# Performance work log

Measured on AMD Instinct MI355X. Metric: run time of the kernel, lower is better.

## Reference

```python
import jax, jax.numpy as jnp
import numpy as np

B, H, W, D, K = 32, 64, 64, 128, 1024

def setup_inputs() -> dict:
    key = jax.random.key(0)
    k1, k2 = jax.random.split(key)
    inputs = jax.random.normal(k1, (B, H, W, D), dtype=jnp.float32)
    embedding = jax.random.normal(k2, (D, K), dtype=jnp.float32)  # codebook, column per code
    return {"inputs": inputs, "embedding": embedding}

def reference(inputs, embedding):
    D_ = embedding.shape[0]
    x = inputs.reshape(-1, D_)                                  # [N, D]
    dist = (jnp.sum(x * x, axis=-1, keepdims=True)
            - 2.0 * (x @ embedding)
            + jnp.sum(embedding * embedding, axis=0, keepdims=True))  # [N, K]
    idx = jnp.argmax(-dist, axis=1).reshape(inputs.shape[:-1])  # [B, H, W]
    return embedding.T[idx]                                     # [B, H, W, D]
```

## Files before the change

kernel.cpp:

```cpp
#include <hip/hip_runtime.h>

#define KC 1024
#define DD 128
#define NT_COUNT (KC / 16)
#define RPB 64

typedef short bf16x8 __attribute__((ext_vector_type(8)));
typedef float f32x4  __attribute__((ext_vector_type(4)));

#define AS1 __attribute__((address_space(1)))
#define AS3 __attribute__((address_space(3)))

static __device__ __forceinline__ unsigned short f2bf(float f) {
    unsigned u = __float_as_uint(f);
    unsigned r = (u + 0x7fffu + ((u >> 16) & 1u)) >> 16;
    return (unsigned short)r;
}
static __device__ __forceinline__ float bf2f(unsigned short h) {
    return __uint_as_float(((unsigned)h) << 16);
}
static __device__ __forceinline__ void gl_lds16(const void* g, void* l) {
    __builtin_amdgcn_global_load_lds((const AS1 void*)g, (AS3 void*)l, 16, 0, 0);
}
static __device__ __forceinline__ void gl_lds4(const void* g, void* l) {
    __builtin_amdgcn_global_load_lds((const AS1 void*)g, (AS3 void*)l, 4, 0, 0);
}

__global__ __launch_bounds__(256) void vq_prep(const float* __restrict__ E,
                                               float* __restrict__ e2h,
                                               float* __restrict__ ET,
                                               unsigned short* __restrict__ Bpk) {
    __shared__ float T[16 * 129];
    const int nt  = blockIdx.x;
    const int tid = threadIdx.x;

    for (int i = tid; i < 16 * DD; i += 256) {
        int d  = i >> 4;
        int kk = i & 15;
        T[kk * 129 + d] = E[(size_t)d * KC + nt * 16 + kk];
    }
    __syncthreads();

    if (tid < 16) {
        float s = 0.f;
#pragma unroll 16
        for (int d = 0; d < DD; ++d) {
            float v = T[tid * 129 + d];
            s = fmaf(v, v, s);
        }
        e2h[nt * 16 + tid] = 512.0f - 0.5f * s;
    }

    for (int i = tid; i < 16 * DD; i += 256) {
        int kk = i >> 7;
        int d  = i & 127;
        ET[(size_t)(nt * 16 + kk) * DD + d] = T[kk * 129 + d];
    }

    {
        const int s    = tid >> 6;
        const int lane = tid & 63;
        const int kk   = lane & 15;
        const int d0   = s * 32 + (lane >> 4) * 8;
        bf16x8 hi, lo;
#pragma unroll
        for (int j = 0; j < 8; ++j) {
            float v = T[kk * 129 + d0 + j];
            unsigned short h = f2bf(v);
            hi[j] = (short)h;
            lo[j] = (short)f2bf(v - bf2f(h));
        }
        char* base = (char*)Bpk + (size_t)nt * 8192 + s * 1024 + lane * 16;
        *(bf16x8*)(base)        = hi;
        *(bf16x8*)(base + 4096) = lo;
    }
}

__global__ __launch_bounds__(64, 2) void vq_main(const float* __restrict__ X,
                                                 const float* __restrict__ e2h,
                                                 const float* __restrict__ ET,
                                                 const unsigned short* __restrict__ Bpk,
                                                 float* __restrict__ Out) {
    __shared__ __align__(16) char lds[2 * 8448];
    int*   s_k1  = (int*)(lds);
    int*   s_k2  = (int*)(lds + 256);
    int*   s_win = (int*)(lds + 512);
    float* s_gap = (float*)(lds + 768);

    const int lane  = threadIdx.x;
    const int quad  = lane >> 4;
    const int n16   = lane & 15;
    const int wrow0 = blockIdx.x * RPB;
    const int lidx16 = lane * 16;
    const int lidx4  = lane * 4;

    bf16x8 ahi[4][4], alo[4][4];
#pragma unroll
    for (int t = 0; t < 4; ++t) {
#pragma unroll
        for (int s = 0; s < 4; ++s) {
            const int row = wrow0 + t * 16 + n16;
            const int d0  = s * 32 + quad * 8;
            const float4 p = *(const float4*)(X + (size_t)row * DD + d0);
            const float4 q = *(const float4*)(X + (size_t)row * DD + d0 + 4);
            float v[8] = {p.x, p.y, p.z, p.w, q.x, q.y, q.z, q.w};
#pragma unroll
            for (int j = 0; j < 8; ++j) {
                unsigned short h = f2bf(v[j]);
                ahi[t][s][j] = (short)h;
                alo[t][s][j] = (short)f2bf(v[j] - bf2f(h));
            }
        }
    }

    float p1[4][4], p2[4][4];
#pragma unroll
    for (int t = 0; t < 4; ++t)
#pragma unroll
        for (int r = 0; r < 4; ++r) { p1[t][r] = 0.0f; p2[t][r] = 0.0f; }

#define STAGE(NT, BOFF)                                                          \
    do {                                                                         \
        const char* g = (const char*)Bpk + (size_t)(NT) * 8192;                  \
        _Pragma("unroll")                                                        \
        for (int c = 0; c < 8; ++c)                                              \
            gl_lds16(g + c * 1024 + lidx16, lds + (BOFF) + c * 1024);            \
        gl_lds4(e2h + (NT) * 16 + n16, lds + (BOFF) + 8192);                     \
    } while (0)

#define TILE(NT, BOFF)                                                           \
    do {                                                                         \
        const char* l = lds + (BOFF);                                            \
        const bf16x8 bh0 = *(const bf16x8*)(l + 0 * 1024 + lidx16);              \
        const bf16x8 bh1 = *(const bf16x8*)(l + 1 * 1024 + lidx16);              \
        const bf16x8 bh2 = *(const bf16x8*)(l + 2 * 1024 + lidx16);              \
        const bf16x8 bh3 = *(const bf16x8*)(l + 3 * 1024 + lidx16);              \
        const bf16x8 bl0 = *(const bf16x8*)(l + 4 * 1024 + lidx16);              \
        const bf16x8 bl1 = *(const bf16x8*)(l + 5 * 1024 + lidx16);              \
        const bf16x8 bl2 = *(const bf16x8*)(l + 6 * 1024 + lidx16);              \
        const bf16x8 bl3 = *(const bf16x8*)(l + 7 * 1024 + lidx16);              \
        const float  ev  = *(const float*)(l + 8192 + lidx4);                    \
        const unsigned ntinv = (unsigned)(63 - (NT));                            \
        _Pragma("unroll")                                                        \
        for (int t = 0; t < 4; ++t) {                                            \
            f32x4 aA = {ev, ev, ev, ev};                                         \
            f32x4 aB = {0.f, 0.f, 0.f, 0.f};                                     \
            f32x4 aC = {0.f, 0.f, 0.f, 0.f};                                     \
            aA = __builtin_amdgcn_mfma_f32_16x16x32_bf16(ahi[t][0], bh0, aA, 0, 0, 0); \
            aB = __builtin_amdgcn_mfma_f32_16x16x32_bf16(alo[t][0], bh0, aB, 0, 0, 0); \
            aC = __builtin_amdgcn_mfma_f32_16x16x32_bf16(ahi[t][0], bl0, aC, 0, 0, 0); \
            aA = __builtin_amdgcn_mfma_f32_16x16x32_bf16(ahi[t][1], bh1, aA, 0, 0, 0); \
            aB = __builtin_amdgcn_mfma_f32_16x16x32_bf16(alo[t][1], bh1, aB, 0, 0, 0); \
            aC = __builtin_amdgcn_mfma_f32_16x16x32_bf16(ahi[t][1], bl1, aC, 0, 0, 0); \
            aA = __builtin_amdgcn_mfma_f32_16x16x32_bf16(ahi[t][2], bh2, aA, 0, 0, 0); \
            aB = __builtin_amdgcn_mfma_f32_16x16x32_bf16(alo[t][2], bh2, aB, 0, 0, 0); \
            aC = __builtin_amdgcn_mfma_f32_16x16x32_bf16(ahi[t][2], bl2, aC, 0, 0, 0); \
            aA = __builtin_amdgcn_mfma_f32_16x16x32_bf16(ahi[t][3], bh3, aA, 0, 0, 0); \
            aB = __builtin_amdgcn_mfma_f32_16x16x32_bf16(alo[t][3], bh3, aB, 0, 0, 0); \
            aC = __builtin_amdgcn_mfma_f32_16x16x32_bf16(ahi[t][3], bl3, aC, 0, 0, 0); \
            _Pragma("unroll")                                                    \
            for (int r = 0; r < 4; ++r) {                                        \
                float sv = (aA[r] + aB[r]) + aC[r];                              \
                float v = __uint_as_float((__float_as_uint(sv) & ~63u) | ntinv); \
                float lo = fminf(p1[t][r], v);                                   \
                p1[t][r] = fmaxf(p1[t][r], v);                                   \
                p2[t][r] = fmaxf(p2[t][r], lo);                                  \
            }                                                                    \
        }                                                                        \
    } while (0)

    STAGE(0, 0);
    for (int nt = 0; nt < NT_COUNT; nt += 2) {
        STAGE(nt + 1, 8448);
        __builtin_amdgcn_s_waitcnt(3961);
        __builtin_amdgcn_sched_barrier(0);
        TILE(nt, 0);
        if (nt + 2 < NT_COUNT) {
            STAGE(nt + 2, 0);
            __builtin_amdgcn_s_waitcnt(3961);
        } else {
            __builtin_amdgcn_s_waitcnt(3952);
        }
        __builtin_amdgcn_sched_barrier(0);
        TILE(nt + 1, 8448);
    }
#undef STAGE
#undef TILE

#pragma unroll
    for (int t = 0; t < 4; ++t) {
#pragma unroll
        for (int r = 0; r < 4; ++r) {
            unsigned u1 = __float_as_uint(p1[t][r]);
            unsigned u2 = __float_as_uint(p2[t][r]);
            int k1 = (int)(63u - (u1 & 63u)) * 16 + n16;
            int k2 = (int)(63u - (u2 & 63u)) * 16 + n16;
            unsigned long long q1 =
                ((unsigned long long)(u1 & ~63u) << 32) | (unsigned)(1023 - k1);
            unsigned long long q2 =
                ((unsigned long long)(u2 & ~63u) << 32) | (unsigned)(1023 - k2);
#pragma unroll
            for (int m = 1; m < 16; m <<= 1) {
                unsigned long long o1 = __shfl_xor(q1, m, 64);
                unsigned long long o2 = __shfl_xor(q2, m, 64);
                unsigned long long lo = q1 < o1 ? q1 : o1;
                q1 = q1 > o1 ? q1 : o1;
                unsigned long long hi2 = q2 > o2 ? q2 : o2;
                q2 = lo > hi2 ? lo : hi2;
            }
            if (n16 == 0) {
                int row = t * 16 + quad * 4 + r;
                s_k1[row] = 1023 - (int)(q1 & 1023u);
                s_k2[row] = 1023 - (int)(q2 & 1023u);
                s_gap[row] = __uint_as_float((unsigned)(q1 >> 32)) -
                             __uint_as_float((unsigned)(q2 >> 32));
            }
        }
    }
    __syncthreads();

    {
        const int k1 = s_k1[lane];
        const int k2 = s_k2[lane];
        int win = k1;
        if (s_gap[lane] < 0.5f) {
            const float4* __restrict__ xr  = (const float4*)(X + (size_t)(wrow0 + lane) * DD);
            const float4* __restrict__ e1  = (const float4*)(ET + (size_t)k1 * DD);
            const float4* __restrict__ e2p = (const float4*)(ET + (size_t)k2 * DD);
            double dot1 = 0.0, ee1 = 0.0, dot2 = 0.0, ee2 = 0.0;
#pragma unroll 4
            for (int d4 = 0; d4 < DD / 4; ++d4) {
                const float4 xv = xr[d4];
                const float4 v1 = e1[d4];
                const float4 v2 = e2p[d4];
                const float xs[4] = {xv.x, xv.y, xv.z, xv.w};
                const float a1[4] = {v1.x, v1.y, v1.z, v1.w};
                const float a2[4] = {v2.x, v2.y, v2.z, v2.w};
#pragma unroll
                for (int j = 0; j < 4; ++j) {
                    const double xd  = (double)xs[j];
                    const double v1d = (double)a1[j];
                    const double v2d = (double)a2[j];
                    dot1 = fma(xd, v1d, dot1);
                    ee1  = fma(v1d, v1d, ee1);
                    dot2 = fma(xd, v2d, dot2);
                    ee2  = fma(v2d, v2d, ee2);
                }
            }
            double d1 = ee1 - 2.0 * dot1;
            double d2 = ee2 - 2.0 * dot2;
            win = (d2 < d1 || (d2 == d1 && k2 < k1)) ? k2 : k1;
        }
        s_win[lane] = win;
    }
    __syncthreads();

    for (int i = lane; i < RPB * (DD / 4); i += 64) {
        const int row = i >> 5;
        const int d4  = i & 31;
        const float4 v = *(const float4*)(ET + (size_t)s_win[row] * DD + d4 * 4);
        *(float4*)(Out + (size_t)(wrow0 + row) * DD + d4 * 4) = v;
    }
}

extern "C" void kernel_launch(void* const* d_in, const int* in_sizes, int n_in,
                              void* d_out, int out_size, void* d_ws, size_t ws_size,
                              hipStream_t stream) {
    const float* X = (const float*)d_in[0];
    const float* E = (const float*)d_in[1];
    float* Out = (float*)d_out;

    float* e2h = (float*)d_ws;
    float* ET  = e2h + KC;
    unsigned short* Bpk = (unsigned short*)(ET + (size_t)KC * DD);

    const int N = in_sizes[0] / DD;

    hipLaunchKernelGGL(vq_prep, dim3(NT_COUNT), dim3(256), 0, stream, E, e2h, ET, Bpk);
    hipLaunchKernelGGL(vq_main, dim3(N / RPB), dim3(64), 0, stream,
                       X, e2h, ET, Bpk, Out);
}
```

Baseline: 216.8 us.

## Triple-buffer codebook tiles, preload code norms into LDS, raise MFMA priority

The main loop moves from double to triple buffering of the packed bf16 codebook tiles, so two tiles are in flight while one is computed, with matching vmcnt waits. The per-tile 4-byte global-to-LDS load of the code norms is replaced by a single upfront copy of all 1024 norms into LDS. s_setprio is raised around the MFMA block. The goal is to hide more global load latency at the cost of extra LDS per block, which could reduce occupancy.

```diff
diff --git a/kernel.cpp b/kernel.cpp
--- a/kernel.cpp
+++ b/kernel.cpp
@@ -11,6 +11,10 @@
 #define AS1 __attribute__((address_space(1)))
 #define AS3 __attribute__((address_space(3)))
 
+#define VMC16 20336
+#define VMC8  3960
+#define VMC0  3952
+
 static __device__ __forceinline__ unsigned short f2bf(float f) {
     unsigned u = __float_as_uint(f);
     unsigned r = (u + 0x7fffu + ((u >> 16) & 1u)) >> 16;
@@ -21,9 +25,6 @@
 }
 static __device__ __forceinline__ void gl_lds16(const void* g, void* l) {
     __builtin_amdgcn_global_load_lds((const AS1 void*)g, (AS3 void*)l, 16, 0, 0);
-}
-static __device__ __forceinline__ void gl_lds4(const void* g, void* l) {
-    __builtin_amdgcn_global_load_lds((const AS1 void*)g, (AS3 void*)l, 4, 0, 0);
 }
 
 __global__ __launch_bounds__(256) void vq_prep(const float* __restrict__ E,
@@ -81,7 +82,8 @@
                                                  const float* __restrict__ ET,
                                                  const unsigned short* __restrict__ Bpk,
                                                  float* __restrict__ Out) {
-    __shared__ __align__(16) char lds[2 * 8448];
+    __shared__ __align__(16) char lds[3 * 8192 + 4096];
+    float* s_e2  = (float*)(lds + 24576);
     int*   s_k1  = (int*)(lds);
     int*   s_k2  = (int*)(lds + 256);
     int*   s_win = (int*)(lds + 512);
@@ -92,7 +94,6 @@
     const int n16   = lane & 15;
     const int wrow0 = blockIdx.x * RPB;
     const int lidx16 = lane * 16;
-    const int lidx4  = lane * 4;
 
     bf16x8 ahi[4][4], alo[4][4];
 #pragma unroll
@@ -113,23 +114,28 @@
         }
     }
 
+    for (int i = lane; i < KC; i += 64) s_e2[i] = e2h[i];
+    __syncthreads();
+
     float p1[4][4], p2[4][4];
 #pragma unroll
     for (int t = 0; t < 4; ++t)
 #pragma unroll
         for (int r = 0; r < 4; ++r) { p1[t][r] = 0.0f; p2[t][r] = 0.0f; }
 
-#define STAGE(NT, BOFF)                                                          \
+#define STAGE(T, BOFF)                                                           \
     do {                                                                         \
-        const char* g = (const char*)Bpk + (size_t)(NT) * 8192;                  \
+        const char* g = (const char*)Bpk + (size_t)(T) * 8192;                   \
         _Pragma("unroll")                                                        \
         for (int c = 0; c < 8; ++c)                                              \
             gl_lds16(g + c * 1024 + lidx16, lds + (BOFF) + c * 1024);            \
-        gl_lds4(e2h + (NT) * 16 + n16, lds + (BOFF) + 8192);                     \
     } while (0)
 
-#define TILE(NT, BOFF)                                                           \
+#define BODY(T, BOFF, STG, SBOFF, WENC)                                          \
     do {                                                                         \
+        if (STG) STAGE((T) + 2, SBOFF);                                          \
+        __builtin_amdgcn_s_waitcnt(WENC);                                        \
+        __builtin_amdgcn_sched_barrier(0);                                       \
         const char* l = lds + (BOFF);                                            \
         const bf16x8 bh0 = *(const bf16x8*)(l + 0 * 1024 + lidx16);              \
         const bf16x8 bh1 = *(const bf16x8*)(l + 1 * 1024 + lidx16);              \
@@ -139,8 +145,9 @@
         const bf16x8 bl1 = *(const bf16x8*)(l + 5 * 1024 + lidx16);              \
         const bf16x8 bl2 = *(const bf16x8*)(l + 6 * 1024 + lidx16);              \
         const bf16x8 bl3 = *(const bf16x8*)(l + 7 * 1024 + lidx16);              \
-        const float  ev  = *(const float*)(l + 8192 + lidx4);                    \
-        const unsigned ntinv = (unsigned)(63 - (NT));                            \
+        const float  ev  = s_e2[(T) * 16 + n16];                                 \
+        const unsigned ntinv = (unsigned)(63 - (T));                             \
+        __builtin_amdgcn_s_setprio(1);                                           \
         _Pragma("unroll")                                                        \
         for (int t = 0; t < 4; ++t) {                                            \
             f32x4 aA = {ev, ev, ev, ev};                                         \
@@ -167,25 +174,22 @@
                 p2[t][r] = fmaxf(p2[t][r], lo);                                  \
             }                                                                    \
         }                                                                        \
+        __builtin_amdgcn_s_setprio(0);                                           \
     } while (0)
 
     STAGE(0, 0);
-    for (int nt = 0; nt < NT_COUNT; nt += 2) {
-        STAGE(nt + 1, 8448);
-        __builtin_amdgcn_s_waitcnt(3961);
-        __builtin_amdgcn_sched_barrier(0);
-        TILE(nt, 0);
-        if (nt + 2 < NT_COUNT) {
-            STAGE(nt + 2, 0);
-            __builtin_amdgcn_s_waitcnt(3961);
-        } else {
-            __builtin_amdgcn_s_waitcnt(3952);
-        }
-        __builtin_amdgcn_sched_barrier(0);
-        TILE(nt + 1, 8448);
-    }
+    STAGE(1, 8192);
+    for (int nt = 0; nt < 60; nt += 3) {
+        BODY(nt,     0,     1, 16384, VMC16);
+        BODY(nt + 1, 8192,  1, 0,     VMC16);
+        BODY(nt + 2, 16384, 1, 8192,  VMC16);
+    }
+    BODY(60, 0,     1, 16384, VMC16);
+    BODY(61, 8192,  1, 0,     VMC16);
+    BODY(62, 16384, 0, 0,     VMC8);
+    BODY(63, 0,     0, 0,     VMC0);
+#undef BODY
 #undef STAGE
-#undef TILE
 
 #pragma unroll
     for (int t = 0; t < 4; ++t) {
```

Measured after the change: 276.4 us. 27.5% more time.

## Load codebook tiles directly into registers instead of async global-to-LDS staging

Applied to the files above, without the earlier changes.

Replaces the global_load_lds double-buffered staging of packed bf16 codebook tiles with plain global loads into two register buffers, leaving the compiler to schedule the waits. The e2 norms are now preloaded once into LDS for all codes rather than staged per tile. This drops the LDS round trip and the manual waitcnt/sched_barrier control, at the cost of 16 extra bf16x8 registers per lane, which may cut occupancy or add spills, and it relies on compiler-inserted waits to overlap loads with the MFMAs.

```diff
diff --git a/kernel.cpp b/kernel.cpp
--- a/kernel.cpp
+++ b/kernel.cpp
@@ -8,9 +8,6 @@
 typedef short bf16x8 __attribute__((ext_vector_type(8)));
 typedef float f32x4  __attribute__((ext_vector_type(4)));
 
-#define AS1 __attribute__((address_space(1)))
-#define AS3 __attribute__((address_space(3)))
-
 static __device__ __forceinline__ unsigned short f2bf(float f) {
     unsigned u = __float_as_uint(f);
     unsigned r = (u + 0x7fffu + ((u >> 16) & 1u)) >> 16;
@@ -18,12 +15,6 @@
 }
 static __device__ __forceinline__ float bf2f(unsigned short h) {
     return __uint_as_float(((unsigned)h) << 16);
-}
-static __device__ __forceinline__ void gl_lds16(const void* g, void* l) {
-    __builtin_amdgcn_global_load_lds((const AS1 void*)g, (AS3 void*)l, 16, 0, 0);
-}
-static __device__ __forceinline__ void gl_lds4(const void* g, void* l) {
-    __builtin_amdgcn_global_load_lds((const AS1 void*)g, (AS3 void*)l, 4, 0, 0);
 }
 
 __global__ __launch_bounds__(256) void vq_prep(const float* __restrict__ E,
@@ -81,18 +72,17 @@
                                                  const float* __restrict__ ET,
                                                  const unsigned short* __restrict__ Bpk,
                                                  float* __restrict__ Out) {
-    __shared__ __align__(16) char lds[2 * 8448];
-    int*   s_k1  = (int*)(lds);
-    int*   s_k2  = (int*)(lds + 256);
-    int*   s_win = (int*)(lds + 512);
-    float* s_gap = (float*)(lds + 768);
+    __shared__ float s_e2[KC];
+    __shared__ int   s_k1[RPB];
+    __shared__ int   s_k2[RPB];
+    __shared__ int   s_win[RPB];
+    __shared__ float s_gap[RPB];
 
     const int lane  = threadIdx.x;
     const int quad  = lane >> 4;
     const int n16   = lane & 15;
     const int wrow0 = blockIdx.x * RPB;
     const int lidx16 = lane * 16;
-    const int lidx4  = lane * 4;
 
     bf16x8 ahi[4][4], alo[4][4];
 #pragma unroll
@@ -113,51 +103,44 @@
         }
     }
 
+    for (int i = lane; i < KC; i += 64) s_e2[i] = e2h[i];
+    __syncthreads();
+
     float p1[4][4], p2[4][4];
 #pragma unroll
     for (int t = 0; t < 4; ++t)
 #pragma unroll
         for (int r = 0; r < 4; ++r) { p1[t][r] = 0.0f; p2[t][r] = 0.0f; }
 
-#define STAGE(NT, BOFF)                                                          \
+#define LOADB(NT, BUF)                                                           \
     do {                                                                         \
-        const char* g = (const char*)Bpk + (size_t)(NT) * 8192;                  \
+        const char* g = (const char*)Bpk + (size_t)(NT) * 8192 + lidx16;         \
         _Pragma("unroll")                                                        \
         for (int c = 0; c < 8; ++c)                                              \
-            gl_lds16(g + c * 1024 + lidx16, lds + (BOFF) + c * 1024);            \
-        gl_lds4(e2h + (NT) * 16 + n16, lds + (BOFF) + 8192);                     \
+            BUF[c] = *(const bf16x8*)(g + c * 1024);                             \
     } while (0)
 
-#define TILE(NT, BOFF)                                                           \
+#define TILE(NT, BUF)                                                            \
     do {                                                                         \
-        const char* l = lds + (BOFF);                                            \
-        const bf16x8 bh0 = *(const bf16x8*)(l + 0 * 1024 + lidx16);              \
-        const bf16x8 bh1 = *(const bf16x8*)(l + 1 * 1024 + lidx16);              \
-        const bf16x8 bh2 = *(const bf16x8*)(l + 2 * 1024 + lidx16);              \
-        const bf16x8 bh3 = *(const bf16x8*)(l + 3 * 1024 + lidx16);              \
-        const bf16x8 bl0 = *(const bf16x8*)(l + 4 * 1024 + lidx16);              \
-        const bf16x8 bl1 = *(const bf16x8*)(l + 5 * 1024 + lidx16);              \
-        const bf16x8 bl2 = *(const bf16x8*)(l + 6 * 1024 + lidx16);              \
-        const bf16x8 bl3 = *(const bf16x8*)(l + 7 * 1024 + lidx16);              \
-        const float  ev  = *(const float*)(l + 8192 + lidx4);                    \
+        const float ev = s_e2[(NT) * 16 + n16];                                  \
         const unsigned ntinv = (unsigned)(63 - (NT));                            \
         _Pragma("unroll")                                                        \
         for (int t = 0; t < 4; ++t) {                                            \
             f32x4 aA = {ev, ev, ev, ev};                                         \
             f32x4 aB = {0.f, 0.f, 0.f, 0.f};                                     \
             f32x4 aC = {0.f, 0.f, 0.f, 0.f};                                     \
-            aA = __builtin_amdgcn_mfma_f32_16x16x32_bf16(ahi[t][0], bh0, aA, 0, 0, 0); \
-            aB = __builtin_amdgcn_mfma_f32_16x16x32_bf16(alo[t][0], bh0, aB, 0, 0, 0); \
-            aC = __builtin_amdgcn_mfma_f32_16x16x32_bf16(ahi[t][0], bl0, aC, 0, 0, 0); \
-            aA = __builtin_amdgcn_mfma_f32_16x16x32_bf16(ahi[t][1], bh1, aA, 0, 0, 0); \
-            aB = __builtin_amdgcn_mfma_f32_16x16x32_bf16(alo[t][1], bh1, aB, 0, 0, 0); \
-            aC = __builtin_amdgcn_mfma_f32_16x16x32_bf16(ahi[t][1], bl1, aC, 0, 0, 0); \
-            aA = __builtin_amdgcn_mfma_f32_16x16x32_bf16(ahi[t][2], bh2, aA, 0, 0, 0); \
-            aB = __builtin_amdgcn_mfma_f32_16x16x32_bf16(alo[t][2], bh2, aB, 0, 0, 0); \
-            aC = __builtin_amdgcn_mfma_f32_16x16x32_bf16(ahi[t][2], bl2, aC, 0, 0, 0); \
-            aA = __builtin_amdgcn_mfma_f32_16x16x32_bf16(ahi[t][3], bh3, aA, 0, 0, 0); \
-            aB = __builtin_amdgcn_mfma_f32_16x16x32_bf16(alo[t][3], bh3, aB, 0, 0, 0); \
-            aC = __builtin_amdgcn_mfma_f32_16x16x32_bf16(ahi[t][3], bl3, aC, 0, 0, 0); \
+            aA = __builtin_amdgcn_mfma_f32_16x16x32_bf16(ahi[t][0], BUF[0], aA, 0, 0, 0); \
+            aB = __builtin_amdgcn_mfma_f32_16x16x32_bf16(alo[t][0], BUF[0], aB, 0, 0, 0); \
+            aC = __builtin_amdgcn_mfma_f32_16x16x32_bf16(ahi[t][0], BUF[4], aC, 0, 0, 0); \
+            aA = __builtin_amdgcn_mfma_f32_16x16x32_bf16(ahi[t][1], BUF[1], aA, 0, 0, 0); \
+            aB = __builtin_amdgcn_mfma_f32_16x16x32_bf16(alo[t][1], BUF[1], aB, 0, 0, 0); \
+            aC = __builtin_amdgcn_mfma_f32_16x16x32_bf16(ahi[t][1], BUF[5], aC, 0, 0, 0); \
+            aA = __builtin_amdgcn_mfma_f32_16x16x32_bf16(ahi[t][2], BUF[2], aA, 0, 0, 0); \
+            aB = __builtin_amdgcn_mfma_f32_16x16x32_bf16(alo[t][2], BUF[2], aB, 0, 0, 0); \
+            aC = __builtin_amdgcn_mfma_f32_16x16x32_bf16(ahi[t][2], BUF[6], aC, 0, 0, 0); \
+            aA = __builtin_amdgcn_mfma_f32_16x16x32_bf16(ahi[t][3], BUF[3], aA, 0, 0, 0); \
+            aB = __builtin_amdgcn_mfma_f32_16x16x32_bf16(alo[t][3], BUF[3], aB, 0, 0, 0); \
+            aC = __builtin_amdgcn_mfma_f32_16x16x32_bf16(ahi[t][3], BUF[7], aC, 0, 0, 0); \
             _Pragma("unroll")                                                    \
             for (int r = 0; r < 4; ++r) {                                        \
                 float sv = (aA[r] + aB[r]) + aC[r];                              \
@@ -169,22 +152,15 @@
         }                                                                        \
     } while (0)
 
-    STAGE(0, 0);
+    bf16x8 bufA[8], bufB[8];
+    LOADB(0, bufA);
     for (int nt = 0; nt < NT_COUNT; nt += 2) {
-        STAGE(nt + 1, 8448);
-        __builtin_amdgcn_s_waitcnt(3961);
-        __builtin_amdgcn_sched_barrier(0);
-        TILE(nt, 0);
-        if (nt + 2 < NT_COUNT) {
-            STAGE(nt + 2, 0);
-            __builtin_amdgcn_s_waitcnt(3961);
-        } else {
-            __builtin_amdgcn_s_waitcnt(3952);
-        }
-        __builtin_amdgcn_sched_barrier(0);
-        TILE(nt + 1, 8448);
-    }
-#undef STAGE
+        LOADB(nt + 1, bufB);
+        TILE(nt, bufA);
+        if (nt + 2 < NT_COUNT) LOADB(nt + 2, bufA);
+        TILE(nt + 1, bufB);
+    }
+#undef LOADB
 #undef TILE
 
 #pragma unroll
```

New measurement: 267.1 us. +23.2%, slower.

## Drop codebook low-part MFMA, use certified top-4 with error-bound rescoring

Applied to the files above, without the earlier changes.

Removes the third bf16 MFMA (x_hi times e_lo) from the split-precision distance product, so each tile issues two MFMA chains instead of three and stages half as much codebook data in LDS. To keep argmin exact, it computes per-tile error bounds on the dropped codebook low part in the prep kernel and keeps a top-4 candidate list per row. A row is accepted only when a gap between consecutive candidates exceeds a bound derived from ||x|| and those error bounds; candidates above the gap are rescored in double precision. Rows that fail all gaps fall back to a full double-precision scan over all 1024 codes. This adds heavier top-4 tracking, a serial per-row candidate merge, and the risk of slow fallbacks.

```diff
diff --git a/kernel.cpp b/kernel.cpp
--- a/kernel.cpp
+++ b/kernel.cpp
@@ -7,6 +7,7 @@
 
 typedef short bf16x8 __attribute__((ext_vector_type(8)));
 typedef float f32x4  __attribute__((ext_vector_type(4)));
+typedef unsigned long long u64;
 
 #define AS1 __attribute__((address_space(1)))
 #define AS3 __attribute__((address_space(3)))
@@ -28,9 +29,11 @@
 
 __global__ __launch_bounds__(256) void vq_prep(const float* __restrict__ E,
                                                float* __restrict__ e2h,
+                                               float* __restrict__ gtab,
                                                float* __restrict__ ET,
                                                unsigned short* __restrict__ Bpk) {
     __shared__ float T[16 * 129];
+    __shared__ float red[32];
     const int nt  = blockIdx.x;
     const int tid = threadIdx.x;
 
@@ -42,13 +45,25 @@
     __syncthreads();
 
     if (tid < 16) {
-        float s = 0.f;
+        float s = 0.f, g = 0.f;
 #pragma unroll 16
         for (int d = 0; d < DD; ++d) {
             float v = T[tid * 129 + d];
             s = fmaf(v, v, s);
+            float lo = v - bf2f(f2bf(v));
+            g = fmaf(lo, lo, g);
         }
         e2h[nt * 16 + tid] = 512.0f - 0.5f * s;
+        red[tid] = g;
+        red[16 + tid] = s;
+    }
+    __syncthreads();
+    if (tid == 0) {
+        float mg = 0.f, ms = 0.f;
+#pragma unroll
+        for (int i = 0; i < 16; ++i) { mg = fmaxf(mg, red[i]); ms = fmaxf(ms, red[16 + i]); }
+        gtab[nt] = mg;
+        gtab[64 + nt] = ms;
     }
 
     for (int i = tid; i < 16 * DD; i += 256) {
@@ -58,34 +73,30 @@
     }
 
     {
-        const int s    = tid >> 6;
+        const int c    = tid >> 6;
         const int lane = tid & 63;
         const int kk   = lane & 15;
-        const int d0   = s * 32 + (lane >> 4) * 8;
-        bf16x8 hi, lo;
-#pragma unroll
-        for (int j = 0; j < 8; ++j) {
-            float v = T[kk * 129 + d0 + j];
-            unsigned short h = f2bf(v);
-            hi[j] = (short)h;
-            lo[j] = (short)f2bf(v - bf2f(h));
-        }
-        char* base = (char*)Bpk + (size_t)nt * 8192 + s * 1024 + lane * 16;
-        *(bf16x8*)(base)        = hi;
-        *(bf16x8*)(base + 4096) = lo;
+        const int d0   = c * 32 + (lane >> 4) * 8;
+        bf16x8 hi;
+#pragma unroll
+        for (int j = 0; j < 8; ++j) hi[j] = (short)f2bf(T[kk * 129 + d0 + j]);
+        *(bf16x8*)((char*)Bpk + (size_t)nt * 4096 + c * 1024 + lane * 16) = hi;
     }
 }
 
 __global__ __launch_bounds__(64, 2) void vq_main(const float* __restrict__ X,
                                                  const float* __restrict__ e2h,
+                                                 const float* __restrict__ gtab,
                                                  const float* __restrict__ ET,
                                                  const unsigned short* __restrict__ Bpk,
                                                  float* __restrict__ Out) {
-    __shared__ __align__(16) char lds[2 * 8448];
-    int*   s_k1  = (int*)(lds);
-    int*   s_k2  = (int*)(lds + 256);
-    int*   s_win = (int*)(lds + 512);
-    float* s_gap = (float*)(lds + 768);
+    __shared__ __align__(16) char lds[11008];
+    float* s_xn   = (float*)(lds + 8704);
+    int*   s_cand = (int*)(lds + 8960);
+    int*   s_dep  = (int*)(lds + 9984);
+    int*   s_win  = (int*)(lds + 10240);
+    int*   s_nfs  = (int*)(lds + 10496);
+    int*   s_fsl  = (int*)(lds + 10500);
 
     const int lane  = threadIdx.x;
     const int quad  = lane >> 4;
@@ -94,7 +105,17 @@
     const int lidx16 = lane * 16;
     const int lidx4  = lane * 4;
 
+    float g1 = gtab[lane];
+    float g2 = gtab[64 + lane];
+#pragma unroll
+    for (int m = 1; m < 64; m <<= 1) {
+        g1 = fmaxf(g1, __shfl_xor(g1, m, 64));
+        g2 = fmaxf(g2, __shfl_xor(g2, m, 64));
+    }
+    const float Ecoef = sqrtf(g1) * 1.001f + 8.2e-6f * sqrtf(g2);
+
     bf16x8 ahi[4][4], alo[4][4];
+    float psum[4] = {0.f, 0.f, 0.f, 0.f};
 #pragma unroll
     for (int t = 0; t < 4; ++t) {
 #pragma unroll
@@ -106,26 +127,36 @@
             float v[8] = {p.x, p.y, p.z, p.w, q.x, q.y, q.z, q.w};
 #pragma unroll
             for (int j = 0; j < 8; ++j) {
+                psum[t] = fmaf(v[j], v[j], psum[t]);
                 unsigned short h = f2bf(v[j]);
                 ahi[t][s][j] = (short)h;
                 alo[t][s][j] = (short)f2bf(v[j] - bf2f(h));
             }
         }
     }
-
-    float p1[4][4], p2[4][4];
+#pragma unroll
+    for (int t = 0; t < 4; ++t) {
+        psum[t] += __shfl_xor(psum[t], 16, 64);
+        psum[t] += __shfl_xor(psum[t], 32, 64);
+    }
+    if (quad == 0)
+#pragma unroll
+        for (int t = 0; t < 4; ++t) s_xn[t * 16 + n16] = psum[t];
+    if (lane == 0) *s_nfs = 0;
+
+    float p1[4][4], p2[4][4], p3[4][4], p4[4][4];
 #pragma unroll
     for (int t = 0; t < 4; ++t)
 #pragma unroll
-        for (int r = 0; r < 4; ++r) { p1[t][r] = 0.0f; p2[t][r] = 0.0f; }
+        for (int r = 0; r < 4; ++r) { p1[t][r] = 0.f; p2[t][r] = 0.f; p3[t][r] = 0.f; p4[t][r] = 0.f; }
 
 #define STAGE(NT, BOFF)                                                          \
     do {                                                                         \
-        const char* g = (const char*)Bpk + (size_t)(NT) * 8192;                  \
+        const char* g = (const char*)Bpk + (size_t)(NT) * 4096;                  \
         _Pragma("unroll")                                                        \
-        for (int c = 0; c < 8; ++c)                                              \
+        for (int c = 0; c < 4; ++c)                                              \
             gl_lds16(g + c * 1024 + lidx16, lds + (BOFF) + c * 1024);            \
-        gl_lds4(e2h + (NT) * 16 + n16, lds + (BOFF) + 8192);                     \
+        gl_lds4(e2h + (NT) * 16 + n16, lds + (BOFF) + 4096);                     \
     } while (0)
 
 #define TILE(NT, BOFF)                                                           \
@@ -135,123 +166,166 @@
         const bf16x8 bh1 = *(const bf16x8*)(l + 1 * 1024 + lidx16);              \
         const bf16x8 bh2 = *(const bf16x8*)(l + 2 * 1024 + lidx16);              \
         const bf16x8 bh3 = *(const bf16x8*)(l + 3 * 1024 + lidx16);              \
-        const bf16x8 bl0 = *(const bf16x8*)(l + 4 * 1024 + lidx16);              \
-        const bf16x8 bl1 = *(const bf16x8*)(l + 5 * 1024 + lidx16);              \
-        const bf16x8 bl2 = *(const bf16x8*)(l + 6 * 1024 + lidx16);              \
-        const bf16x8 bl3 = *(const bf16x8*)(l + 7 * 1024 + lidx16);              \
-        const float  ev  = *(const float*)(l + 8192 + lidx4);                    \
+        const float  ev  = *(const float*)(l + 4096 + lidx4);                    \
         const unsigned ntinv = (unsigned)(63 - (NT));                            \
         _Pragma("unroll")                                                        \
         for (int t = 0; t < 4; ++t) {                                            \
             f32x4 aA = {ev, ev, ev, ev};                                         \
             f32x4 aB = {0.f, 0.f, 0.f, 0.f};                                     \
-            f32x4 aC = {0.f, 0.f, 0.f, 0.f};                                     \
             aA = __builtin_amdgcn_mfma_f32_16x16x32_bf16(ahi[t][0], bh0, aA, 0, 0, 0); \
             aB = __builtin_amdgcn_mfma_f32_16x16x32_bf16(alo[t][0], bh0, aB, 0, 0, 0); \
-            aC = __builtin_amdgcn_mfma_f32_16x16x32_bf16(ahi[t][0], bl0, aC, 0, 0, 0); \
             aA = __builtin_amdgcn_mfma_f32_16x16x32_bf16(ahi[t][1], bh1, aA, 0, 0, 0); \
             aB = __builtin_amdgcn_mfma_f32_16x16x32_bf16(alo[t][1], bh1, aB, 0, 0, 0); \
-            aC = __builtin_amdgcn_mfma_f32_16x16x32_bf16(ahi[t][1], bl1, aC, 0, 0, 0); \
             aA = __builtin_amdgcn_mfma_f32_16x16x32_bf16(ahi[t][2], bh2, aA, 0, 0, 0); \
             aB = __builtin_amdgcn_mfma_f32_16x16x32_bf16(alo[t][2], bh2, aB, 0, 0, 0); \
-            aC = __builtin_amdgcn_mfma_f32_16x16x32_bf16(ahi[t][2], bl2, aC, 0, 0, 0); \
             aA = __builtin_amdgcn_mfma_f32_16x16x32_bf16(ahi[t][3], bh3, aA, 0, 0, 0); \
             aB = __builtin_amdgcn_mfma_f32_16x16x32_bf16(alo[t][3], bh3, aB, 0, 0, 0); \
-            aC = __builtin_amdgcn_mfma_f32_16x16x32_bf16(ahi[t][3], bl3, aC, 0, 0, 0); \
             _Pragma("unroll")                                                    \
             for (int r = 0; r < 4; ++r) {                                        \
-                float sv = (aA[r] + aB[r]) + aC[r];                              \
+                float sv = aA[r] + aB[r];                                        \
                 float v = __uint_as_float((__float_as_uint(sv) & ~63u) | ntinv); \
-                float lo = fminf(p1[t][r], v);                                   \
-                p1[t][r] = fmaxf(p1[t][r], v);                                   \
-                p2[t][r] = fmaxf(p2[t][r], lo);                                  \
+                float t1 = fmaxf(p1[t][r], v), b1 = fminf(p1[t][r], v);          \
+                float t2 = fmaxf(p2[t][r], b1), b2 = fminf(p2[t][r], b1);        \
+                float t3 = fmaxf(p3[t][r], b2), b3 = fminf(p3[t][r], b2);        \
+                p4[t][r] = fmaxf(p4[t][r], b3);                                  \
+                p1[t][r] = t1; p2[t][r] = t2; p3[t][r] = t3;                     \
             }                                                                    \
         }                                                                        \
     } while (0)
 
     STAGE(0, 0);
     for (int nt = 0; nt < NT_COUNT; nt += 2) {
-        STAGE(nt + 1, 8448);
-        __builtin_amdgcn_s_waitcnt(3961);
+        STAGE(nt + 1, 4352);
+        __builtin_amdgcn_s_waitcnt(3957);
         __builtin_amdgcn_sched_barrier(0);
         TILE(nt, 0);
         if (nt + 2 < NT_COUNT) {
             STAGE(nt + 2, 0);
-            __builtin_amdgcn_s_waitcnt(3961);
+            __builtin_amdgcn_s_waitcnt(3957);
         } else {
             __builtin_amdgcn_s_waitcnt(3952);
         }
         __builtin_amdgcn_sched_barrier(0);
-        TILE(nt + 1, 8448);
+        TILE(nt + 1, 4352);
     }
 #undef STAGE
 #undef TILE
 
-#pragma unroll
-    for (int t = 0; t < 4; ++t) {
+    u64* dmp = (u64*)lds;
+    for (int ph = 0; ph < 4; ++ph) {
+        __syncthreads();
 #pragma unroll
         for (int r = 0; r < 4; ++r) {
-            unsigned u1 = __float_as_uint(p1[t][r]);
-            unsigned u2 = __float_as_uint(p2[t][r]);
-            int k1 = (int)(63u - (u1 & 63u)) * 16 + n16;
-            int k2 = (int)(63u - (u2 & 63u)) * 16 + n16;
-            unsigned long long q1 =
-                ((unsigned long long)(u1 & ~63u) << 32) | (unsigned)(1023 - k1);
-            unsigned long long q2 =
-                ((unsigned long long)(u2 & ~63u) << 32) | (unsigned)(1023 - k2);
-#pragma unroll
-            for (int m = 1; m < 16; m <<= 1) {
-                unsigned long long o1 = __shfl_xor(q1, m, 64);
-                unsigned long long o2 = __shfl_xor(q2, m, 64);
-                unsigned long long lo = q1 < o1 ? q1 : o1;
-                q1 = q1 > o1 ? q1 : o1;
-                unsigned long long hi2 = q2 > o2 ? q2 : o2;
-                q2 = lo > hi2 ? lo : hi2;
-            }
-            if (n16 == 0) {
-                int row = t * 16 + quad * 4 + r;
-                s_k1[row] = 1023 - (int)(q1 & 1023u);
-                s_k2[row] = 1023 - (int)(q2 & 1023u);
-                s_gap[row] = __uint_as_float((unsigned)(q1 >> 32)) -
-                             __uint_as_float((unsigned)(q2 >> 32));
-            }
+            float pp[4] = {p1[ph][r], p2[ph][r], p3[ph][r], p4[ph][r]};
+            u64* base = dmp + (quad * 4 + r) * 64 + n16 * 4;
+#pragma unroll
+            for (int j = 0; j < 4; ++j) {
+                unsigned u = __float_as_uint(pp[j]);
+                int k = (int)(63u - (u & 63u)) * 16 + n16;
+                base[j] = ((u64)(u & ~63u) << 32) | (unsigned)(1023 - k);
+            }
+        }
+        __syncthreads();
+        if (lane < 16) {
+            const u64* c = dmp + lane * 64;
+            u64 q1 = 0, q2 = 0, q3 = 0, q4 = 0;
+#pragma unroll 8
+            for (int i = 0; i < 64; ++i) {
+                u64 v = c[i];
+                u64 t1 = v > q1 ? v : q1, b1 = v > q1 ? q1 : v;
+                u64 t2 = b1 > q2 ? b1 : q2, b2 = b1 > q2 ? q2 : b1;
+                u64 t3 = b2 > q3 ? b2 : q3, b3 = b2 > q3 ? q3 : b2;
+                q4 = b3 > q4 ? b3 : q4; q1 = t1; q2 = t2; q3 = t3;
+            }
+            const int row = ph * 16 + lane;
+            const float v1 = __uint_as_float((unsigned)(q1 >> 32));
+            const float v2 = __uint_as_float((unsigned)(q2 >> 32));
+            const float v3 = __uint_as_float((unsigned)(q3 >> 32));
+            const float v4 = __uint_as_float((unsigned)(q4 >> 32));
+            const float xn = sqrtf(s_xn[row]) * 1.0001f;
+            const float TRIG = 2.0f * (xn * Ecoef + 0.008f) + 1e-4f;
+            int dep = (v1 - v2 >= TRIG) ? 1 :
+                      (v2 - v3 >= TRIG) ? 2 :
+                      (v3 - v4 >= TRIG) ? 3 : 0;
+            s_cand[row * 4 + 0] = 1023 - (int)(q1 & 1023u);
+            s_cand[row * 4 + 1] = 1023 - (int)(q2 & 1023u);
+            s_cand[row * 4 + 2] = 1023 - (int)(q3 & 1023u);
+            s_cand[row * 4 + 3] = 1023 - (int)(q4 & 1023u);
+            s_dep[row] = dep;
+            if (dep == 0) { int idx = atomicAdd(s_nfs, 1); s_fsl[idx] = row; }
         }
     }
     __syncthreads();
 
     {
-        const int k1 = s_k1[lane];
-        const int k2 = s_k2[lane];
-        int win = k1;
-        if (s_gap[lane] < 0.5f) {
-            const float4* __restrict__ xr  = (const float4*)(X + (size_t)(wrow0 + lane) * DD);
-            const float4* __restrict__ e1  = (const float4*)(ET + (size_t)k1 * DD);
-            const float4* __restrict__ e2p = (const float4*)(ET + (size_t)k2 * DD);
-            double dot1 = 0.0, ee1 = 0.0, dot2 = 0.0, ee2 = 0.0;
+        const int dep = s_dep[lane];
+        int win = s_cand[lane * 4];
+        if (dep >= 2) {
+            const float4* __restrict__ xr = (const float4*)(X + (size_t)(wrow0 + lane) * DD);
+            double bestd = 1.0e300; int bestk = 0x7fffffff;
+            for (int j = 0; j < 3; ++j) {
+                if (j >= dep) break;
+                const int k = s_cand[lane * 4 + j];
+                const float4* __restrict__ ep = (const float4*)(ET + (size_t)k * DD);
+                double dot = 0.0, ee = 0.0;
 #pragma unroll 4
-            for (int d4 = 0; d4 < DD / 4; ++d4) {
-                const float4 xv = xr[d4];
-                const float4 v1 = e1[d4];
-                const float4 v2 = e2p[d4];
-                const float xs[4] = {xv.x, xv.y, xv.z, xv.w};
-                const float a1[4] = {v1.x, v1.y, v1.z, v1.w};
-                const float a2[4] = {v2.x, v2.y, v2.z, v2.w};
-#pragma unroll
-                for (int j = 0; j < 4; ++j) {
-                    const double xd  = (double)xs[j];
-                    const double v1d = (double)a1[j];
-                    const double v2d = (double)a2[j];
-                    dot1 = fma(xd, v1d, dot1);
-                    ee1  = fma(v1d, v1d, ee1);
-                    dot2 = fma(xd, v2d, dot2);
-                    ee2  = fma(v2d, v2d, ee2);
+                for (int d4 = 0; d4 < DD / 4; ++d4) {
+                    const float4 xv = xr[d4];
+                    const float4 evv = ep[d4];
+                    const float xs[4] = {xv.x, xv.y, xv.z, xv.w};
+                    const float es[4] = {evv.x, evv.y, evv.z, evv.w};
+#pragma unroll
+                    for (int jj = 0; jj < 4; ++jj) {
+                        const double xd = (double)xs[jj];
+                        const double ed = (double)es[jj];
+                        dot = fma(xd, ed, dot);
+                        ee  = fma(ed, ed, ee);
+                    }
                 }
-            }
-            double d1 = ee1 - 2.0 * dot1;
-            double d2 = ee2 - 2.0 * dot2;
-            win = (d2 < d1 || (d2 == d1 && k2 < k1)) ? k2 : k1;
-        }
-        s_win[lane] = win;
+                const double dd = ee - 2.0 * dot;
+                if (dd < bestd || (dd == bestd && k < bestk)) { bestd = dd; bestk = k; }
+            }
+            win = bestk;
+        }
+        if (dep != 0) s_win[lane] = win;
+    }
+    __syncthreads();
+
+    {
+        const int n = *s_nfs;
+        for (int i = 0; i < n; ++i) {
+            const int row = s_fsl[i];
+            const float4* __restrict__ xr = (const float4*)(X + (size_t)(wrow0 + row) * DD);
+            double bestd = 1.0e300; int bestk = 0x7fffffff;
+            for (int c = 0; c < 16; ++c) {
+                const int k = c * 64 + lane;
+                const float4* __restrict__ ep = (const float4*)(ET + (size_t)k * DD);
+                double dot = 0.0, ee = 0.0;
+#pragma unroll 8
+                for (int d4 = 0; d4 < DD / 4; ++d4) {
+                    const float4 xv = xr[d4];
+                    const float4 evv = ep[d4];
+                    const float xs[4] = {xv.x, xv.y, xv.z, xv.w};
+                    const float es[4] = {evv.x, evv.y, evv.z, evv.w};
+#pragma unroll
+                    for (int jj = 0; jj < 4; ++jj) {
+                        const double xd = (double)xs[jj];
+                        const double ed = (double)es[jj];
+                        dot = fma(xd, ed, dot);
+                        ee  = fma(ed, ed, ee);
+                    }
+                }
+                const double dd = ee - 2.0 * dot;
+                if (dd < bestd || (dd == bestd && k < bestk)) { bestd = dd; bestk = k; }
+            }
+#pragma unroll
+            for (int m = 1; m < 64; m <<= 1) {
+                const double od = __shfl_xor(bestd, m, 64);
+                const int    ok = __shfl_xor(bestk, m, 64);
+                if (od < bestd || (od == bestd && ok < bestk)) { bestd = od; bestk = ok; }
+            }
+            if (lane == 0) s_win[row] = bestk;
+        }
     }
     __syncthreads();
 
@@ -270,13 +344,14 @@
     const float* E = (const float*)d_in[1];
     float* Out = (float*)d_out;
 
-    float* e2h = (float*)d_ws;
-    float* ET  = e2h + KC;
+    float* e2h  = (float*)d_ws;
+    float* gtab = e2h + KC;
+    float* ET   = gtab + 128;
     unsigned short* Bpk = (unsigned short*)(ET + (size_t)KC * DD);
 
     const int N = in_sizes[0] / DD;
 
-    hipLaunchKernelGGL(vq_prep, dim3(NT_COUNT), dim3(256), 0, stream, E, e2h, ET, Bpk);
+    hipLaunchKernelGGL(vq_prep, dim3(NT_COUNT), dim3(256), 0, stream, E, e2h, gtab, ET, Bpk);
     hipLaunchKernelGGL(vq_main, dim3(N / RPB), dim3(64), 0, stream,
-                       X, e2h, ET, Bpk, Out);
-}
+                       X, e2h, gtab, ET, Bpk, Out);
+}
```

Result: slower. 571.5 us (+163.6%).
